# Kernel tuning notes

Hardware: AMD Instinct MI355X
Metric: run time of the kernel (lower is better)

The kernel has to match this reference:

```python
import jax, jax.numpy as jnp
import numpy as np

N = 100000   # nodes
R = 3        # relation types (num_edge_type)
E = 600000   # edges per relation -> Etot = 1.8M
C = 2        # num_channels
L = 2        # num_layers (GTConv stack / metapath length)
IN = 64      # in_dim
H = 64       # hidden_dim
K = 50       # num_class
NEG_SLOPE = 0.2  # DGL GATConv default leaky_relu slope


def setup_inputs() -> dict:
    key = jax.random.key(0)
    ks = jax.random.split(key, 12)
    Etot = R * E
    src = jax.random.randint(ks[0], (Etot,), 0, N)
    dst = jax.random.randint(ks[1], (Etot,), 0, N)
    rel = jnp.repeat(jnp.arange(R), E)  # relation id per edge
    h = jax.random.normal(ks[2], (N, IN), jnp.float32)
    # per-channel input projections (fastGTN self.params, xavier-ish)
    params = jax.random.normal(ks[3], (C, IN, H), jnp.float32) * (1.0 / np.sqrt(IN))
    # GTConv weights, one [C, R] filter per layer (init std=0.01)
    gt_w = jax.random.normal(ks[4], (L, C, R), jnp.float32) * 0.01
    # GATConv params: fc (no bias), attn_l, attn_r (num_heads=1)
    fc_w = jax.random.normal(ks[5], (H, H), jnp.float32) * (1.0 / np.sqrt(H))
    attn_l = jax.random.normal(ks[6], (H,), jnp.float32) * 0.1
    attn_r = jax.random.normal(ks[7], (H,), jnp.float32) * 0.1
    # linear_weights: Embedding initialized to 1/top_k, combines channels
    lin_w = jnp.full((C,), 1.0 / C, jnp.float32)
    W2 = jax.random.normal(ks[8], (H, K), jnp.float32) * (1.0 / np.sqrt(H))
    b2 = jnp.zeros((K,), jnp.float32)
    return dict(h=h, params=params, gt_w=gt_w, fc_w=fc_w, attn_l=attn_l,
                attn_r=attn_r, lin_w=lin_w, W2=W2, b2=b2,
                src=src, dst=dst, rel=rel)


def _segment_softmax(logits, seg, n):
    # numerically stable edge softmax over incoming edges of each dst node
    m = jax.ops.segment_max(logits, seg, num_segments=n)
    e = jnp.exp(logits - m[seg])
    s = jax.ops.segment_sum(e, seg, num_segments=n)
    return e / s[seg]


def _gat(src, dst, ft, ew, attn_l, attn_r, n):
    # GATConv_Grad: attention from original ft, then two update_all passes
    el = ft @ attn_l                                   # [N]
    er = ft @ attn_r                                   # [N]
    logits = jax.nn.leaky_relu(el[src] + er[dst], NEG_SLOPE)
    a = _segment_softmax(logits, dst, n)               # [Etot]
    # pass 1: ft <- sum_e ft[src]*edge_weight  (overwrites node frame 'ft')
    ft1 = jax.ops.segment_sum(ft[src] * ew[:, None], dst, num_segments=n)
    # pass 2: ft <- sum_e ft1[src]*a
    ft2 = jax.ops.segment_sum(ft1[src] * a[:, None], dst, num_segments=n)
    return ft2


def reference(h, params, gt_w, fc_w, attn_l, attn_r, lin_w, W2, b2, src, dst, rel):
    n = h.shape[0]
    outs = []
    for c in range(params.shape[0]):           # num_channels (small, fixed)
        Hc = h @ params[c]                     # [N, H]
        for l in range(gt_w.shape[0]):         # num_layers (small, fixed)
            filt = jax.nn.softmax(gt_w[l], axis=-1)     # [C, R] GTConv softmax
            w_e = filt[c][rel]                           # combined relation-graph edge weight
            # EdgeWeightNorm('right'): divide by weighted in-degree at dst
            deg = jax.ops.segment_sum(w_e, dst, num_segments=n)
            w_norm = w_e / jnp.where(deg[dst] > 0, deg[dst], 1.0)
            ft = Hc @ fc_w                               # GAT fc projection
            Hc = _gat(src, dst, ft, w_norm, attn_l, attn_r, n)
        outs.append(Hc)
    Hm = jnp.einsum('c,cnd->nd', lin_w, jnp.stack(outs, 0))  # linear_weights combine
    return Hm @ W2 + b2                        # linear2 -> class logits [N, K]
```

## Files before the change

### kernel.cpp

```cpp
#include <hip/hip_runtime.h>
#include <hip/hip_bf16.h>
#include <hip/hip_fp16.h>
#include <math.h>

#define NEG_SLOPE 0.2f
#define NPB_SHIFT 7
#define NPB 128
#define SC_EDGES 16384
#define MAXD 128

__device__ __forceinline__ unsigned hpack(float a, float b) {
    __half2 h = __floats2half2_rn(a, b);
    return *(unsigned*)&h;
}
__device__ __forceinline__ float2 hunpack(unsigned v) {
    __half2 h = *(__half2*)&v;
    return make_float2(__low2float(h), __high2float(h));
}
__device__ __forceinline__ void fmix_lo(float& acc, unsigned v, unsigned w) {
    asm("v_fma_mix_f32 %0, %1, %2, %0 op_sel:[0,0,0] op_sel_hi:[1,1,0]"
        : "+v"(acc) : "v"(v), "v"(w));
}
__device__ __forceinline__ void fmix_hi(float& acc, unsigned v, unsigned w) {
    asm("v_fma_mix_f32 %0, %1, %2, %0 op_sel:[1,1,0] op_sel_hi:[1,1,0]"
        : "+v"(acc) : "v"(v), "v"(w));
}

__global__ void mkfilt(const float* __restrict__ gt_w, float* __restrict__ filt,
                       int rows) {
    int i = threadIdx.x;
    if (i < rows) {
        const float* g = gt_w + i * 3;
        float m = fmaxf(g[0], fmaxf(g[1], g[2]));
        float e0 = __expf(g[0] - m), e1 = __expf(g[1] - m), e2 = __expf(g[2] - m);
        float s = e0 + e1 + e2;
        filt[i * 3 + 0] = e0 / s;
        filt[i * 3 + 1] = e1 / s;
        filt[i * 3 + 2] = e2 / s;
    }
}

__global__ __launch_bounds__(256) void combw_kernel(const float* __restrict__ params,
                                                    const float* __restrict__ fc_w,
                                                    float* __restrict__ WcF) {
    __shared__ __align__(16) float sP[64 * 64], sF[64 * 64];
    const float* P = params + (size_t)blockIdx.x * 64 * 64;
    int t = threadIdx.x;
    for (int i = t * 4; i < 4096; i += 1024) {
        *(float4*)&sP[i] = *(const float4*)&P[i];
        *(float4*)&sF[i] = *(const float4*)&fc_w[i];
    }
    __syncthreads();
    float* O = WcF + (size_t)blockIdx.x * 64 * 64;
    for (int i = t; i < 4096; i += 256) {
        int r = i >> 6, c = i & 63;
        float acc = 0.f;
#pragma unroll
        for (int k = 0; k < 64; ++k) acc += sP[r * 64 + k] * sF[k * 64 + c];
        O[i] = acc;
    }
}

__global__ __launch_bounds__(256) void prep2_kernel(const float* __restrict__ fc_w,
                                                    const float* __restrict__ W2,
                                                    const float* __restrict__ attn_l,
                                                    const float* __restrict__ attn_r,
                                                    float* __restrict__ WfcW2,
                                                    float2* __restrict__ wlr) {
    __shared__ __align__(16) float sF[4096];
    __shared__ float sW[3200], sal[64], sar[64];
    int t = threadIdx.x;
    for (int i = t * 4; i < 4096; i += 1024)
        *(float4*)&sF[i] = *(const float4*)&fc_w[i];
    for (int i = t; i < 3200; i += 256) sW[i] = W2[i];
    if (t < 64) { sal[t] = attn_l[t]; sar[t] = attn_r[t]; }
    __syncthreads();
    if (t < 64) {
        float l = 0.f, r = 0.f;
#pragma unroll
        for (int k = 0; k < 64; ++k) {
            l += sF[t * 64 + k] * sal[k];
            r += sF[t * 64 + k] * sar[k];
        }
        wlr[t] = make_float2(l, r);
    }
    for (int i = t; i < 3200; i += 256) {
        int r = i / 50, c = i - r * 50;
        float acc = 0.f;
#pragma unroll
        for (int k = 0; k < 64; ++k) acc += sF[r * 64 + k] * sW[k * 50 + c];
        WfcW2[i] = acc;
    }
}

__global__ __launch_bounds__(256) void bcount_kernel(const int* __restrict__ dst,
                                                     int* __restrict__ bcnt, int m, int NB) {
    __shared__ int h[1024];
    for (int i = threadIdx.x; i < NB; i += 256) h[i] = 0;
    __syncthreads();
    int base = blockIdx.x * SC_EDGES;
    int endi = base + SC_EDGES; if (endi > m) endi = m;
    for (int i = base + threadIdx.x; i < endi; i += 256)
        atomicAdd(&h[dst[i] >> NPB_SHIFT], 1);
    __syncthreads();
    for (int i = threadIdx.x; i < NB; i += 256)
        if (h[i]) atomicAdd(&bcnt[i], h[i]);
}

__global__ __launch_bounds__(1024) void bscan_kernel(const int* __restrict__ bcnt,
                                                     int* __restrict__ bbase,
                                                     int* __restrict__ bcur, int NB) {
    __shared__ int s[1024];
    int t = threadIdx.x;
    int v = (t < NB) ? bcnt[t] : 0;
    s[t] = v;
    __syncthreads();
    for (int off = 1; off < 1024; off <<= 1) {
        int u = (t >= off) ? s[t - off] : 0;
        __syncthreads();
        s[t] += u;
        __syncthreads();
    }
    if (t < NB) { bbase[t] = s[t] - v; bcur[t] = s[t] - v; }
    if (t == 1023) bbase[NB] = s[1023];
}

__global__ __launch_bounds__(256) void bscatter_kernel(const int* __restrict__ src,
                                                       const int* __restrict__ dst,
                                                       const int* __restrict__ rel,
                                                       int* __restrict__ bcur,
                                                       unsigned* __restrict__ ebuf,
                                                       int m, int NB) {
    __shared__ int cnt[1024];
    for (int i = threadIdx.x; i < NB; i += 256) cnt[i] = 0;
    __syncthreads();
    int base = blockIdx.x * SC_EDGES;
    int endi = base + SC_EDGES; if (endi > m) endi = m;
    for (int i = base + threadIdx.x; i < endi; i += 256)
        atomicAdd(&cnt[dst[i] >> NPB_SHIFT], 1);
    __syncthreads();
    for (int b = threadIdx.x; b < NB; b += 256) {
        int c = cnt[b];
        if (c) cnt[b] = atomicAdd(&bcur[b], c);
    }
    __syncthreads();
    for (int i = base + threadIdx.x; i < endi; i += 256) {
        int d = dst[i];
        int bk = d >> NPB_SHIFT;
        unsigned pk = (unsigned)src[i] | ((unsigned)rel[i] << 17) |
                      ((unsigned)(d & (NPB - 1)) << 19);
        int pos = atomicAdd(&cnt[bk], 1);
        ebuf[pos] = pk;
    }
}

__global__ __launch_bounds__(256) void bfinal_kernel(const unsigned* __restrict__ ebuf,
                                                     const int* __restrict__ bbase,
                                                     int* __restrict__ rowp,
                                                     unsigned* __restrict__ csr,
                                                     int n, int m, int NB) {
    __shared__ int cnt[NPB], cur[NPB], sc[NPB];
    int b = blockIdx.x;
    int t = threadIdx.x;
    int e0 = bbase[b], e1 = bbase[b + 1];
    if (t < NPB) cnt[t] = 0;
    __syncthreads();
    for (int j = e0 + t; j < e1; j += 256)
        atomicAdd(&cnt[(ebuf[j] >> 19) & (NPB - 1)], 1);
    __syncthreads();
    int v0 = (t < NPB) ? cnt[t] : 0;
    if (t < NPB) sc[t] = v0;
    __syncthreads();
    for (int off = 1; off < NPB; off <<= 1) {
        int u = (t >= off && t < NPB) ? sc[t - off] : 0;
        __syncthreads();
        if (t < NPB) sc[t] += u;
        __syncthreads();
    }
    if (t < NPB) {
        int ex = e0 + sc[t] - v0;
        cur[t] = ex;
        int v = b * NPB + t;
        if (v < n) rowp[v] = ex;
    }
    if (b == 0 && t == 0) rowp[n] = m;
    __syncthreads();
    for (int j = e0 + t; j < e1; j += 256) {
        unsigned pk = ebuf[j];
        int dl = (pk >> 19) & (NPB - 1);
        int pos = atomicAdd(&cur[dl], 1);
        csr[pos] = (pk & 0x1FFFF) | (((pk >> 17) & 3) << 20);
    }
}

__global__ __launch_bounds__(256) void gemm_f0(const float* __restrict__ A,
                                               const float* __restrict__ WcF,
                                               unsigned* __restrict__ OAB, int n,
                                               const float* __restrict__ attn_l,
                                               const float* __restrict__ attn_r,
                                               float2* __restrict__ el2,
                                               float2* __restrict__ er2) {
    __shared__ __align__(16) float sW[2][64 * 64];
    __shared__ __align__(16) float sA[64 * 68];
    __shared__ float sAl[64], sAr[64];
    int t = threadIdx.x;
    int row0 = blockIdx.x * 64;
    for (int i = t * 4; i < 8192; i += 1024)
        *(float4*)&sW[0][i] = *(const float4*)&WcF[i];
    if (t < 64) { sAl[t] = attn_l[t]; sAr[t] = attn_r[t]; }
    int rows = n - row0; if (rows > 64) rows = 64;
    for (int i = t * 4; i < 4096; i += 1024) {
        int r = i >> 6, c = i & 63;
        float4 v = {0.f, 0.f, 0.f, 0.f};
        if (r < rows) v = *(const float4*)&A[(size_t)(row0 + r) * 64 + c];
        *(float4*)&sA[r * 68 + c] = v;
    }
    __syncthreads();
    int tr = (t >> 4) * 4, tc = (t & 15) * 4;
    float accA[4][4] = {}, accB[4][4] = {};
#pragma unroll 4
    for (int k = 0; k < 64; k += 4) {
        float4 av[4];
#pragma unroll
        for (int i = 0; i < 4; ++i) av[i] = *(const float4*)&sA[(tr + i) * 68 + k];
#pragma unroll
        for (int kk = 0; kk < 4; ++kk) {
            float4 bA = *(const float4*)&sW[0][(k + kk) * 64 + tc];
            float4 bB = *(const float4*)&sW[1][(k + kk) * 64 + tc];
#pragma unroll
            for (int i = 0; i < 4; ++i) {
                float a = (&av[i].x)[kk];
                accA[i][0] += a * bA.x; accA[i][1] += a * bA.y;
                accA[i][2] += a * bA.z; accA[i][3] += a * bA.w;
                accB[i][0] += a * bB.x; accB[i][1] += a * bB.y;
                accB[i][2] += a * bB.z; accB[i][3] += a * bB.w;
            }
        }
    }
#pragma unroll
    for (int i = 0; i < 4; ++i) {
        int r = row0 + tr + i;
        if (r < n) {
            uint4 v = {hpack(accA[i][0], accB[i][0]), hpack(accA[i][1], accB[i][1]),
                       hpack(accA[i][2], accB[i][2]), hpack(accA[i][3], accB[i][3])};
            *(uint4*)&OAB[(size_t)r * 64 + tc] = v;
        }
    }
    float plA[4], prA[4], plB[4], prB[4];
#pragma unroll
    for (int i = 0; i < 4; ++i) {
        float la = 0.f, ra = 0.f, lb = 0.f, rb = 0.f;
#pragma unroll
        for (int j = 0; j < 4; ++j) {
            la += accA[i][j] * sAl[tc + j]; ra += accA[i][j] * sAr[tc + j];
            lb += accB[i][j] * sAl[tc + j]; rb += accB[i][j] * sAr[tc + j];
        }
        plA[i] = la; prA[i] = ra; plB[i] = lb; prB[i] = rb;
    }
#pragma unroll
    for (int off = 1; off < 16; off <<= 1) {
#pragma unroll
        for (int i = 0; i < 4; ++i) {
            plA[i] += __shfl_xor(plA[i], off); prA[i] += __shfl_xor(prA[i], off);
            plB[i] += __shfl_xor(plB[i], off); prB[i] += __shfl_xor(prB[i], off);
        }
    }
    if ((t & 15) == 0) {
#pragma unroll
        for (int i = 0; i < 4; ++i) {
            int r = row0 + tr + i;
            if (r < n) {
                el2[r] = make_float2(plA[i], plB[i]);
                er2[r] = make_float2(prA[i], prB[i]);
            }
        }
    }
}

__global__ __launch_bounds__(256) void agg1_ab(
        const int* __restrict__ rowp, const unsigned* __restrict__ csr,
        const float* __restrict__ filt, int fo0, int fo1,
        const float2* __restrict__ el, const float2* __restrict__ er,
        const unsigned* __restrict__ ftAB, unsigned* __restrict__ oAB,
        unsigned* __restrict__ ab, float2* __restrict__ sb, int n) {
    __shared__ uint2 sPW[4][MAXD];
    int w = (blockIdx.x * blockDim.x + threadIdx.x) >> 6;
    int lane = threadIdx.x & 63;
    int wv = threadIdx.x >> 6;
    if (w >= n) return;
    int base = rowp[w], end = rowp[w + 1];
    float fA0 = filt[fo0], fA1 = filt[fo0 + 1], fA2 = filt[fo0 + 2];
    float fB0 = filt[fo1], fB1 = filt[fo1 + 1], fB2 = filt[fo1 + 2];
    float2 erv = er[w];
    const char* ftb = (const char*)ftAB;
    unsigned laneoff = (unsigned)lane << 2;

    float degA = 0.f, degB = 0.f, ssA = 0.f, ssB = 0.f;
    for (int j = base + lane; j < end; j += 64) {
        unsigned pk = csr[j];
        int d = j - base;
        int s = pk & 0x1FFFF;
        int r = pk >> 20;
        float wA = (r == 0) ? fA0 : ((r == 1) ? fA1 : fA2);
        float wB = (r == 0) ? fB0 : ((r == 1) ? fB1 : fB2);
        if (d < MAXD) sPW[wv][d] = make_uint2(pk, hpack(wA, wB));
        degA += wA; degB += wB;
        float2 e2 = el[s];
        float xA = e2.x + erv.x;
        float eA = __expf(xA > 0.f ? xA : NEG_SLOPE * xA);
        float xB = e2.y + erv.y;
        float eB = __expf(xB > 0.f ? xB : NEG_SLOPE * xB);
        ab[j] = hpack(eA, eB);
        ssA += eA; ssB += eB;
    }
    for (int off = 32; off; off >>= 1) {
        degA += __shfl_xor(degA, off); degB += __shfl_xor(degB, off);
        ssA += __shfl_xor(ssA, off);   ssB += __shfl_xor(ssB, off);
    }
    float dA = degA > 0.f ? degA : 1.f;
    float dB = degB > 0.f ? degB : 1.f;

    int deg = end - base;
    int dmax = deg < MAXD ? deg : MAXD;
    float accA = 0.f, accB = 0.f;
    int jj = 0;
    for (; jj + 8 <= dmax; jj += 8) {
        uint2 p0 = sPW[wv][jj],     p1 = sPW[wv][jj + 1];
        uint2 p2 = sPW[wv][jj + 2], p3 = sPW[wv][jj + 3];
        uint2 p4 = sPW[wv][jj + 4], p5 = sPW[wv][jj + 5];
        uint2 p6 = sPW[wv][jj + 6], p7 = sPW[wv][jj + 7];
        unsigned v0 = *(const unsigned*)(ftb + (((p0.x & 0x1FFFF) << 8) + laneoff));
        unsigned v1 = *(const unsigned*)(ftb + (((p1.x & 0x1FFFF) << 8) + laneoff));
        unsigned v2 = *(const unsigned*)(ftb + (((p2.x & 0x1FFFF) << 8) + laneoff));
        unsigned v3 = *(const unsigned*)(ftb + (((p3.x & 0x1FFFF) << 8) + laneoff));
        unsigned v4 = *(const unsigned*)(ftb + (((p4.x & 0x1FFFF) << 8) + laneoff));
        unsigned v5 = *(const unsigned*)(ftb + (((p5.x & 0x1FFFF) << 8) + laneoff));
        unsigned v6 = *(const unsigned*)(ftb + (((p6.x & 0x1FFFF) << 8) + laneoff));
        unsigned v7 = *(const unsigned*)(ftb + (((p7.x & 0x1FFFF) << 8) + laneoff));
        fmix_lo(accA, v0, p0.y); fmix_hi(accB, v0, p0.y);
        fmix_lo(accA, v1, p1.y); fmix_hi(accB, v1, p1.y);
        fmix_lo(accA, v2, p2.y); fmix_hi(accB, v2, p2.y);
        fmix_lo(accA, v3, p3.y); fmix_hi(accB, v3, p3.y);
        fmix_lo(accA, v4, p4.y); fmix_hi(accB, v4, p4.y);
        fmix_lo(accA, v5, p5.y); fmix_hi(accB, v5, p5.y);
        fmix_lo(accA, v6, p6.y); fmix_hi(accB, v6, p6.y);
        fmix_lo(accA, v7, p7.y); fmix_hi(accB, v7, p7.y);
    }
    for (; jj < dmax; ++jj) {
        uint2 p = sPW[wv][jj];
        unsigned v = *(const unsigned*)(ftb + (((p.x & 0x1FFFF) << 8) + laneoff));
        fmix_lo(accA, v, p.y); fmix_hi(accB, v, p.y);
    }
    for (int j = base + MAXD; j < end; ++j) {
        unsigned pk = csr[j];
        int s = pk & 0x1FFFF;
        int r = pk >> 20;
        float2 v = hunpack(*(const unsigned*)(ftb + ((unsigned)(s << 8) + laneoff)));
        accA += ((r == 0) ? fA0 : ((r == 1) ? fA1 : fA2)) * v.x;
        accB += ((r == 0) ? fB0 : ((r == 1) ? fB1 : fB2)) * v.y;
    }
    oAB[(size_t)w * 64 + lane] = hpack(accA / dA, accB / dB);
    if (lane == 0)
        sb[w] = make_float2(ssA > 0.f ? 1.f / ssA : 0.f,
                            ssB > 0.f ? 1.f / ssB : 0.f);
}

template <bool EPI>
__global__ __launch_bounds__(256) void agg2_ab(
        const int* __restrict__ rowp, const unsigned* __restrict__ csr,
        const unsigned* __restrict__ ab, const float2* __restrict__ sb,
        const unsigned* __restrict__ ftAB, unsigned* __restrict__ oAB,
        const float2* __restrict__ wlr,
        float2* __restrict__ elout, float2* __restrict__ erout, int n) {
    __shared__ uint2 sPW[4][MAXD];
    __shared__ float2 sWlr[64];
    int t = threadIdx.x;
    if (EPI) {
        if (t < 64) sWlr[t] = wlr[t];
        __syncthreads();
    }
    int w = (blockIdx.x * blockDim.x + t) >> 6;
    int lane = t & 63;
    int wv = t >> 6;
    if (w >= n) return;
    int base = rowp[w], end = rowp[w + 1];
    float2 inv = sb[w];
    const char* ftb = (const char*)ftAB;
    unsigned laneoff = (unsigned)lane << 2;

    for (int j = base + lane; j < end; j += 64) {
        int d = j - base;
        if (d < MAXD) sPW[wv][d] = make_uint2(csr[j], ab[j]);
    }

    int deg = end - base;
    int dmax = deg < MAXD ? deg : MAXD;
    float accA = 0.f, accB = 0.f;
    int jj = 0;
    for (; jj + 8 <= dmax; jj += 8) {
        uint2 p0 = sPW[wv][jj],     p1 = sPW[wv][jj + 1];
        uint2 p2 = sPW[wv][jj + 2], p3 = sPW[wv][jj + 3];
        uint2 p4 = sPW[wv][jj + 4], p5 = sPW[wv][jj + 5];
        uint2 p6 = sPW[wv][jj + 6], p7 = sPW[wv][jj + 7];
        unsigned v0 = *(const unsigned*)(ftb + (((p0.x & 0x1FFFF) << 8) + laneoff));
        unsigned v1 = *(const unsigned*)(ftb + (((p1.x & 0x1FFFF) << 8) + laneoff));
        unsigned v2 = *(const unsigned*)(ftb + (((p2.x & 0x1FFFF) << 8) + laneoff));
        unsigned v3 = *(const unsigned*)(ftb + (((p3.x & 0x1FFFF) << 8) + laneoff));
        unsigned v4 = *(const unsigned*)(ftb + (((p4.x & 0x1FFFF) << 8) + laneoff));
        unsigned v5 = *(const unsigned*)(ftb + (((p5.x & 0x1FFFF) << 8) + laneoff));
        unsigned v6 = *(const unsigned*)(ftb + (((p6.x & 0x1FFFF) << 8) + laneoff));
        unsigned v7 = *(const unsigned*)(ftb + (((p7.x & 0x1FFFF) << 8) + laneoff));
        fmix_lo(accA, v0, p0.y); fmix_hi(accB, v0, p0.y);
        fmix_lo(accA, v1, p1.y); fmix_hi(accB, v1, p1.y);
        fmix_lo(accA, v2, p2.y); fmix_hi(accB, v2, p2.y);
        fmix_lo(accA, v3, p3.y); fmix_hi(accB, v3, p3.y);
        fmix_lo(accA, v4, p4.y); fmix_hi(accB, v4, p4.y);
        fmix_lo(accA, v5, p5.y); fmix_hi(accB, v5, p5.y);
        fmix_lo(accA, v6, p6.y); fmix_hi(accB, v6, p6.y);
        fmix_lo(accA, v7, p7.y); fmix_hi(accB, v7, p7.y);
    }
    for (; jj < dmax; ++jj) {
        uint2 p = sPW[wv][jj];
        unsigned v = *(const unsigned*)(ftb + (((p.x & 0x1FFFF) << 8) + laneoff));
        fmix_lo(accA, v, p.y); fmix_hi(accB, v, p.y);
    }
    for (int j = base + MAXD; j < end; ++j) {
        unsigned pk = csr[j];
        int s = pk & 0x1FFFF;
        float2 ev = hunpack(ab[j]);
        float2 v = hunpack(*(const unsigned*)(ftb + ((unsigned)(s << 8) + laneoff)));
        accA += ev.x * v.x;
        accB += ev.y * v.y;
    }
    float oA = accA * inv.x, oB = accB * inv.y;
    oAB[(size_t)w * 64 + lane] = hpack(oA, oB);
    if (EPI) {
        float2 wv2 = sWlr[lane];
        float elA = oA * wv2.x, elB = oB * wv2.x;
        float erA = oA * wv2.y, erB = oB * wv2.y;
        for (int off = 32; off; off >>= 1) {
            elA += __shfl_xor(elA, off); elB += __shfl_xor(elB, off);
            erA += __shfl_xor(erA, off); erB += __shfl_xor(erB, off);
        }
        if (lane == 0) {
            elout[w] = make_float2(elA, elB);
            erout[w] = make_float2(erA, erB);
        }
    }
}

__global__ __launch_bounds__(256) void gemm_out_ab(const unsigned* __restrict__ AAB,
                                                   const float* __restrict__ W,
                                                   const float* __restrict__ b2,
                                                   const float* __restrict__ lin_w,
                                                   float* __restrict__ out, int n) {
    __shared__ __align__(16) float sW[64 * 50];
    __shared__ __align__(16) float sA[64 * 68];
    int t = threadIdx.x;
    int row0 = blockIdx.x * 64;
    float lw0 = lin_w[0], lw1 = lin_w[1];
    for (int i = t; i < 64 * 50; i += 256) sW[i] = W[i];
    int rows = n - row0; if (rows > 64) rows = 64;
    for (int i = t * 4; i < 4096; i += 1024) {
        int r = i >> 6, c = i & 63;
        uint4 v = {0u, 0u, 0u, 0u};
        if (r < rows) v = *(const uint4*)&AAB[(size_t)(row0 + r) * 64 + c];
        float2 f0 = hunpack(v.x), f1 = hunpack(v.y);
        float2 f2 = hunpack(v.z), f3 = hunpack(v.w);
        sA[r * 68 + c]     = lw0 * f0.x + lw1 * f0.y;
        sA[r * 68 + c + 1] = lw0 * f1.x + lw1 * f1.y;
        sA[r * 68 + c + 2] = lw0 * f2.x + lw1 * f2.y;
        sA[r * 68 + c + 3] = lw0 * f3.x + lw1 * f3.y;
    }
    __syncthreads();
    for (int i = t; i < 64 * 50; i += 256) {
        int r = i / 50, col = i - r * 50;
        if (row0 + r >= n) continue;
        float acc = 0.f;
#pragma unroll
        for (int k = 0; k < 64; ++k) acc += sA[r * 68 + k] * sW[k * 50 + col];
        out[(size_t)(row0 + r) * 50 + col] = b2[col] + acc;
    }
}

extern "C" void kernel_launch(void* const* d_in, const int* in_sizes, int n_in,
                              void* d_out, int out_size, void* d_ws, size_t ws_size,
                              hipStream_t stream) {
    const float* h      = (const float*)d_in[0];
    const float* params = (const float*)d_in[1];
    const float* gt_w   = (const float*)d_in[2];
    const float* fc_w   = (const float*)d_in[3];
    const float* attn_l = (const float*)d_in[4];
    const float* attn_r = (const float*)d_in[5];
    const float* lin_w  = (const float*)d_in[6];
    const float* W2     = (const float*)d_in[7];
    const float* b2     = (const float*)d_in[8];
    const int*   src    = (const int*)d_in[9];
    const int*   dst    = (const int*)d_in[10];
    const int*   rel    = (const int*)d_in[11];

    const int n = in_sizes[0] / 64;
    const int m = in_sizes[9];
    const int C = 2, L = 2;
    float* out = (float*)d_out;

    char* base = (char*)d_ws;
    size_t off = 0;
    auto alloc = [&](size_t bytes) -> char* {
        char* p = base + off;
        off = (off + bytes + 255) & ~(size_t)255;
        return p;
    };
    const int NB = (n + NPB - 1) >> NPB_SHIFT;
    const int nchunks = (m + SC_EDGES - 1) / SC_EDGES;
    float*    filt  = (float*)alloc(L * C * 3 * sizeof(float));
    float*    WcF   = (float*)alloc((size_t)C * 64 * 64 * 4);
    float*    WfcW2 = (float*)alloc((size_t)64 * 50 * 4);
    float2*   wlr   = (float2*)alloc((size_t)64 * 8);
    int*      bcnt  = (int*)alloc((size_t)NB * 4);
    int*      bbase = (int*)alloc((size_t)(NB + 1) * 4);
    int*      bcur  = (int*)alloc((size_t)NB * 4);
    int*      rowp  = (int*)alloc((size_t)(n + 1) * 4);
    unsigned* ebuf  = (unsigned*)alloc((size_t)m * 4);
    unsigned* csr   = (unsigned*)alloc((size_t)m * 4);
    unsigned* abuf  = (unsigned*)alloc((size_t)m * 4);
    float2*   el1   = (float2*)alloc((size_t)n * 8);
    float2*   er1   = (float2*)alloc((size_t)n * 8);
    float2*   elL2  = (float2*)alloc((size_t)n * 8);
    float2*   erL2  = (float2*)alloc((size_t)n * 8);
    float2*   sbAB  = (float2*)alloc((size_t)n * 8);
    unsigned* FAB   = (unsigned*)alloc((size_t)n * 64 * 4);
    unsigned* GAB   = (unsigned*)alloc((size_t)n * 64 * 4);
    unsigned* HAB   = (unsigned*)alloc((size_t)n * 64 * 4);

    hipMemsetAsync(bcnt, 0, (size_t)NB * 4, stream);
    mkfilt<<<1, 64, 0, stream>>>(gt_w, filt, L * C);
    combw_kernel<<<C, 256, 0, stream>>>(params, fc_w, WcF);
    prep2_kernel<<<1, 256, 0, stream>>>(fc_w, W2, attn_l, attn_r, WfcW2, wlr);
    bcount_kernel<<<nchunks, 256, 0, stream>>>(dst, bcnt, m, NB);
    bscan_kernel<<<1, 1024, 0, stream>>>(bcnt, bbase, bcur, NB);
    bscatter_kernel<<<nchunks, 256, 0, stream>>>(src, dst, rel, bcur, ebuf, m, NB);
    bfinal_kernel<<<NB, 256, 0, stream>>>(ebuf, bbase, rowp, csr, n, m, NB);

    const int gB = (n + 63) / 64;
    const int waveBlocks = (n + 3) / 4;

    gemm_f0<<<gB, 256, 0, stream>>>(h, WcF, FAB, n, attn_l, attn_r, el1, er1);
    agg1_ab<<<waveBlocks, 256, 0, stream>>>(rowp, csr, filt, 0, 3,
                                            el1, er1, FAB, GAB, abuf, sbAB, n);
    agg2_ab<true><<<waveBlocks, 256, 0, stream>>>(rowp, csr, abuf, sbAB,
                                                  GAB, HAB, wlr, elL2, erL2, n);
    agg1_ab<<<waveBlocks, 256, 0, stream>>>(rowp, csr, filt, 6, 9,
                                            elL2, erL2, HAB, GAB, abuf, sbAB, n);
    agg2_ab<false><<<waveBlocks, 256, 0, stream>>>(rowp, csr, abuf, sbAB,
                                                   GAB, HAB, nullptr, nullptr, nullptr, n);
    gemm_out_ab<<<gB, 256, 0, stream>>>(HAB, WfcW2, b2, lin_w, out, n);
}
```

Baseline: 472.9 us.

## Store per-chunk bucket histograms to skip recount and global atomics in scatter

```diff
diff --git a/kernel.cpp b/kernel.cpp
--- a/kernel.cpp
+++ b/kernel.cpp
@@ -6,7 +6,7 @@
 #define NEG_SLOPE 0.2f
 #define NPB_SHIFT 7
 #define NPB 128
-#define SC_EDGES 16384
+#define SC_EDGES 65536
 #define MAXD 128
 
 __device__ __forceinline__ unsigned hpack(float a, float b) {
@@ -94,7 +94,9 @@
 }
 
 __global__ __launch_bounds__(256) void bcount_kernel(const int* __restrict__ dst,
-                                                     int* __restrict__ bcnt, int m, int NB) {
+                                                     int* __restrict__ bcnt,
+                                                     int* __restrict__ blockhist,
+                                                     int m, int NB) {
     __shared__ int h[1024];
     for (int i = threadIdx.x; i < NB; i += 256) h[i] = 0;
     __syncthreads();
@@ -103,13 +105,18 @@
     for (int i = base + threadIdx.x; i < endi; i += 256)
         atomicAdd(&h[dst[i] >> NPB_SHIFT], 1);
     __syncthreads();
-    for (int i = threadIdx.x; i < NB; i += 256)
-        if (h[i]) atomicAdd(&bcnt[i], h[i]);
+    int* bh = blockhist + (size_t)blockIdx.x * NB;
+    for (int i = threadIdx.x; i < NB; i += 256) {
+        int c = h[i];
+        bh[i] = c;
+        if (c) atomicAdd(&bcnt[i], c);
+    }
 }
 
 __global__ __launch_bounds__(1024) void bscan_kernel(const int* __restrict__ bcnt,
                                                      int* __restrict__ bbase,
-                                                     int* __restrict__ bcur, int NB) {
+                                                     int* __restrict__ blockhist,
+                                                     int NB, int nchunks) {
     __shared__ int s[1024];
     int t = threadIdx.x;
     int v = (t < NB) ? bcnt[t] : 0;
@@ -121,29 +128,32 @@
         s[t] += u;
         __syncthreads();
     }
-    if (t < NB) { bbase[t] = s[t] - v; bcur[t] = s[t] - v; }
+    if (t < NB) bbase[t] = s[t] - v;
     if (t == 1023) bbase[NB] = s[1023];
+    __syncthreads();
+    if (t < NB) {
+        int run = s[t] - v;
+        for (int blk = 0; blk < nchunks; ++blk) {
+            int* p = blockhist + (size_t)blk * NB + t;
+            int c = *p;
+            *p = run;
+            run += c;
+        }
+    }
 }
 
 __global__ __launch_bounds__(256) void bscatter_kernel(const int* __restrict__ src,
                                                        const int* __restrict__ dst,
                                                        const int* __restrict__ rel,
-                                                       int* __restrict__ bcur,
+                                                       const int* __restrict__ blockhist,
                                                        unsigned* __restrict__ ebuf,
                                                        int m, int NB) {
     __shared__ int cnt[1024];
-    for (int i = threadIdx.x; i < NB; i += 256) cnt[i] = 0;
+    const int* bh = blockhist + (size_t)blockIdx.x * NB;
+    for (int i = threadIdx.x; i < NB; i += 256) cnt[i] = bh[i];
     __syncthreads();
     int base = blockIdx.x * SC_EDGES;
     int endi = base + SC_EDGES; if (endi > m) endi = m;
-    for (int i = base + threadIdx.x; i < endi; i += 256)
-        atomicAdd(&cnt[dst[i] >> NPB_SHIFT], 1);
-    __syncthreads();
-    for (int b = threadIdx.x; b < NB; b += 256) {
-        int c = cnt[b];
-        if (c) cnt[b] = atomicAdd(&bcur[b], c);
-    }
-    __syncthreads();
     for (int i = base + threadIdx.x; i < endi; i += 256) {
         int d = dst[i];
         int bk = d >> NPB_SHIFT;
@@ -519,7 +529,7 @@
     float2*   wlr   = (float2*)alloc((size_t)64 * 8);
     int*      bcnt  = (int*)alloc((size_t)NB * 4);
     int*      bbase = (int*)alloc((size_t)(NB + 1) * 4);
-    int*      bcur  = (int*)alloc((size_t)NB * 4);
+    int*      bhist = (int*)alloc((size_t)nchunks * NB * 4);
     int*      rowp  = (int*)alloc((size_t)(n + 1) * 4);
     unsigned* ebuf  = (unsigned*)alloc((size_t)m * 4);
     unsigned* csr   = (unsigned*)alloc((size_t)m * 4);
@@ -537,9 +547,9 @@
     mkfilt<<<1, 64, 0, stream>>>(gt_w, filt, L * C);
     combw_kernel<<<C, 256, 0, stream>>>(params, fc_w, WcF);
     prep2_kernel<<<1, 256, 0, stream>>>(fc_w, W2, attn_l, attn_r, WfcW2, wlr);
-    bcount_kernel<<<nchunks, 256, 0, stream>>>(dst, bcnt, m, NB);
-    bscan_kernel<<<1, 1024, 0, stream>>>(bcnt, bbase, bcur, NB);
-    bscatter_kernel<<<nchunks, 256, 0, stream>>>(src, dst, rel, bcur, ebuf, m, NB);
+    bcount_kernel<<<nchunks, 256, 0, stream>>>(dst, bcnt, bhist, m, NB);
+    bscan_kernel<<<1, 1024, 0, stream>>>(bcnt, bbase, bhist, NB, nchunks);
+    bscatter_kernel<<<nchunks, 256, 0, stream>>>(src, dst, rel, bhist, ebuf, m, NB);
     bfinal_kernel<<<NB, 256, 0, stream>>>(ebuf, bbase, rowp, csr, n, m, NB);
 
     const int gB = (n + 63) / 64;
```

Result: slower. 578.6 us, median of 4 (+22.3%).
